# Kernel tuning notes

Measured on AMD Instinct MI355X. Metric: run time of the kernel, lower is better.

## Reference

```python
import jax, jax.numpy as jnp
import numpy as np

N_STATE = 1024
N_HEAD = 16
HEAD_DIM = N_STATE // N_HEAD
SCALE = HEAD_DIM ** (-0.25)


def setup_inputs() -> dict:
    key = jax.random.key(0)
    ks = jax.random.split(key, 9)
    B, S, D = 32, 1500, N_STATE
    std = 1.0 / np.sqrt(D)
    return {
        "hidden_states": jax.random.normal(ks[0], (B, 1, D), dtype=jnp.float32),
        "encoder_output": jax.random.normal(ks[1], (B, S, D), dtype=jnp.float32),
        "Wq": jax.random.normal(ks[2], (D, D), dtype=jnp.float32) * std,
        "bq": jax.random.normal(ks[3], (D,), dtype=jnp.float32) * std,
        "Wk": jax.random.normal(ks[4], (D, D), dtype=jnp.float32) * std,
        "Wv": jax.random.normal(ks[5], (D, D), dtype=jnp.float32) * std,
        "bv": jax.random.normal(ks[6], (D,), dtype=jnp.float32) * std,
        "Wo": jax.random.normal(ks[7], (D, D), dtype=jnp.float32) * std,
        "bo": jax.random.normal(ks[8], (D,), dtype=jnp.float32) * std,
    }


def reference(hidden_states, encoder_output, Wq, bq, Wk, Wv, bv, Wo, bo):
    B = hidden_states.shape[0]
    S = encoder_output.shape[1]
    # projections (torch F.linear: x @ W.T + b)
    q = hidden_states @ Wq.T + bq                  # [B, 1, D]
    k_original = encoder_output @ Wk.T             # [B, S, D] (no bias)
    v_original = encoder_output @ Wv.T + bv        # [B, S, D]

    q = q.reshape(B, 1, N_HEAD, HEAD_DIM).transpose(0, 2, 1, 3)         # [B,H,1,hd]
    k = k_original.reshape(B, S, N_HEAD, HEAD_DIM).transpose(0, 2, 1, 3)  # [B,H,S,hd]
    v = v_original.reshape(B, S, N_HEAD, HEAD_DIM).transpose(0, 2, 1, 3)  # [B,H,S,hd]

    # pre-scaled q and k, scores in fp32 softmax then cast back
    attn_weights = jnp.einsum('bhqd,bhkd->bhqk', q * SCALE, k * SCALE)  # [B,H,1,S]
    attn_weights = jax.nn.softmax(attn_weights.astype(jnp.float32), axis=-1).astype(q.dtype)
    attn_output = jnp.einsum('bhqk,bhkd->bhqd', attn_weights, v)        # [B,H,1,hd]
    attn_output = attn_output.transpose(0, 2, 1, 3).reshape(B, 1, N_STATE)
    attn_output = attn_output @ Wo.T + bo
    return attn_output, k_original, v_original
```

## Files before the change

kernel.cpp:

```cpp
#include <hip/hip_runtime.h>
#include <cstdint>
#include <cstddef>

#define D_MODEL 1024
#define NH      16
#define HD      64
#define B_SZ    32
#define SEQ     1500
#define MROWS   (B_SZ * SEQ)
#define KD      1024
#define NCH     16
#define PSTR    68

typedef __attribute__((ext_vector_type(8))) short bf16x8;
typedef __attribute__((ext_vector_type(4))) float f32x4;
typedef unsigned short u16;

__device__ __forceinline__ u16 f2b(float f) {
  unsigned int x = __float_as_uint(f);
  x = (x + 0x7FFFu + ((x >> 16) & 1u)) >> 16;
  return (u16)x;
}

#define ENC_BLOCKS 3000
#define W_BLOCKS   64
#define QPROJ_BLOCKS 64

__global__ __launch_bounds__(256) void cast_all_q(const float* __restrict__ enc,
                                                  const float* __restrict__ Wk,
                                                  const float* __restrict__ Wv,
                                                  const float* __restrict__ hs,
                                                  const float* __restrict__ Wq,
                                                  const float* __restrict__ bq,
                                                  u16* __restrict__ encb,
                                                  u16* __restrict__ wkvb,
                                                  float* __restrict__ qs) {
  const int tid = threadIdx.x;
  const int bid = blockIdx.x;
  if (bid < ENC_BLOCKS) {
    const float4* s4 = (const float4*)enc;
    const size_t base = (size_t)bid * 256 + tid;
    #pragma unroll
    for (int k = 0; k < 16; ++k) {
      size_t i = base + (size_t)k * (ENC_BLOCKS * 256);
      float4 a = s4[i];
      u16 u[4] = { f2b(a.x), f2b(a.y), f2b(a.z), f2b(a.w) };
      *reinterpret_cast<uint2*>(encb + i * 4) = *reinterpret_cast<const uint2*>(u);
    }
  } else if (bid < ENC_BLOCKS + W_BLOCKS) {
    const int wb = bid - ENC_BLOCKS;
    const size_t base = (size_t)wb * 256 + tid;
    const int NW4 = KD * KD / 4;
    #pragma unroll
    for (int k = 0; k < 32; ++k) {
      size_t i = base + (size_t)k * (W_BLOCKS * 256);
      const float4* s4 = (i < (size_t)NW4) ? (const float4*)Wk : (const float4*)Wv;
      size_t j = (i < (size_t)NW4) ? i : i - NW4;
      float4 a = s4[j];
      u16 u[4] = { f2b(a.x), f2b(a.y), f2b(a.z), f2b(a.w) };
      *reinterpret_cast<uint2*>(wkvb + i * 4) = *reinterpret_cast<const uint2*>(u);
    }
  } else {
    const int qb = bid - ENC_BLOCKS - W_BLOCKS;
    const int n  = qb * 16 + (tid & 15);
    const int bb = tid >> 4;
    const float4* wp  = (const float4*)(Wq + (size_t)n * D_MODEL);
    const float4* x0p = (const float4*)(hs + (size_t)bb * D_MODEL);
    const float4* x1p = (const float4*)(hs + (size_t)(bb + 16) * D_MODEL);
    float a0 = 0.f, a1 = 0.f;
    #pragma unroll 8
    for (int i = 0; i < D_MODEL / 4; ++i) {
      float4 w = wp[i], x0 = x0p[i], x1 = x1p[i];
      a0 += w.x * x0.x + w.y * x0.y + w.z * x0.z + w.w * x0.w;
      a1 += w.x * x1.x + w.y * x1.y + w.z * x1.z + w.w * x1.w;
    }
    const float bqn = bq[n];
    qs[(size_t)bb * D_MODEL + n]        = (a0 + bqn) * 0.125f;
    qs[(size_t)(bb + 16) * D_MODEL + n] = (a1 + bqn) * 0.125f;
  }
}

#define GBM 128
#define GBN 256
#define GBK 32
#define GNT (KD / GBK)
#define AT  (GBM * GBK)
#define BT  (GBN * GBK)

__device__ __forceinline__ void stageA(const u16* __restrict__ Ag, u16* lbuf,
                                       long m0, int kt, int tid) {
  int c = tid;
  int r = c >> 2, cp = c & 3;
  int scp = cp ^ ((r >> 1) & 3);
  const u16* src = Ag + (m0 + r) * (long)KD + kt * GBK + scp * 8;
  __builtin_amdgcn_global_load_lds((const __attribute__((address_space(1))) void*)src,
      (__attribute__((address_space(3))) void*)(lbuf + (size_t)c * 8), 16, 0, 0);
}

__device__ __forceinline__ void stageB(const u16* __restrict__ Bg, u16* lbuf,
                                       int n0, int kt, int tid) {
  #pragma unroll
  for (int L = 0; L < 2; ++L) {
    int c = tid + L * 512;
    int r = c >> 2, cp = c & 3;
    int scp = cp ^ ((r >> 1) & 3);
    const u16* src = Bg + (size_t)(n0 + r) * KD + kt * GBK + scp * 8;
    __builtin_amdgcn_global_load_lds((const __attribute__((address_space(1))) void*)src,
        (__attribute__((address_space(3))) void*)(lbuf + (size_t)c * 8), 16, 0, 0);
  }
}

__device__ __forceinline__ bf16x8 ldFrag(const u16* buf, int row, int lane) {
  int r  = row + (lane & 15);
  int ch = (lane >> 4) ^ ((r >> 1) & 3);
  return *(const bf16x8*)(buf + (size_t)r * GBK + ch * 8);
}

__global__ __launch_bounds__(512, 4) void gemm_kv(const u16* __restrict__ A,
                                                  const u16* __restrict__ Bm,
                                                  const float* __restrict__ bv,
                                                  float* __restrict__ Kout,
                                                  float* __restrict__ Vout) {
  __shared__ __align__(16) char smem[3 * (GBM + GBN) * GBK * 2];
  u16* sAb = (u16*)smem;
  u16* sBb = sAb + 3 * AT;

  const int tid  = threadIdx.x;
  const int lane = tid & 63;
  const int wid  = tid >> 6;
  const int wr   = wid >> 2;
  const int wc   = wid & 3;

  int bx = (blockIdx.x & 7) * (gridDim.x >> 3) + (blockIdx.x >> 3);
  const int  mt = bx >> 3;
  const int  nt = bx & 7;
  const long m0 = (long)mt * GBM;
  const int  n0 = nt * GBN;

  stageA(A, sAb + 0 * AT, m0, 0, tid);
  stageB(Bm, sBb + 0 * BT, n0, 0, tid);
  stageA(A, sAb + 1 * AT, m0, 1, tid);
  stageB(Bm, sBb + 1 * BT, n0, 1, tid);
  stageA(A, sAb + 2 * AT, m0, 2, tid);
  stageB(Bm, sBb + 2 * BT, n0, 2, tid);

  f32x4 acc[4][4] = {};

  for (int t = 0; t < GNT; ++t) {
    if (t < GNT - 2)       { asm volatile("s_waitcnt vmcnt(6)" ::: "memory"); }
    else if (t == GNT - 2) { asm volatile("s_waitcnt vmcnt(3)" ::: "memory"); }
    else                   { asm volatile("s_waitcnt vmcnt(0)" ::: "memory"); }
    __builtin_amdgcn_s_barrier();

    const int  bi = t % 3;
    const u16* cA = sAb + bi * AT;
    const u16* cB = sBb + bi * BT;
    bf16x8 af[4], bfr[4];
    #pragma unroll
    for (int mf = 0; mf < 4; ++mf) af[mf]  = ldFrag(cA, wr * 64 + mf * 16, lane);
    #pragma unroll
    for (int nf = 0; nf < 4; ++nf) bfr[nf] = ldFrag(cB, wc * 64 + nf * 16, lane);
    asm volatile("s_waitcnt lgkmcnt(0)" ::: "memory");
    __builtin_amdgcn_s_barrier();

    if (t + 3 < GNT) {
      stageA(A, sAb + bi * AT, m0, t + 3, tid);
      stageB(Bm, sBb + bi * BT, n0, t + 3, tid);
    }

    #pragma unroll
    for (int mf = 0; mf < 4; ++mf)
      #pragma unroll
      for (int nf = 0; nf < 4; ++nf)
        acc[mf][nf] = __builtin_amdgcn_mfma_f32_16x16x32_bf16(af[mf], bfr[nf], acc[mf][nf], 0, 0, 0);
  }

  __syncthreads();
  float (*ep)[260] = (float(*)[260])smem;

  const bool isV = (nt >= 4);
  float* Co = isV ? Vout : Kout;
  const int ncol0 = isV ? (n0 - 1024) : n0;
  float4 bias4[4];
  #pragma unroll
  for (int k = 0; k < 4; ++k) {
    int c4 = (tid + 512 * k) & 63;
    bias4[k] = isV ? reinterpret_cast<const float4*>(bv)[(ncol0 >> 2) + c4]
                   : make_float4(0.f, 0.f, 0.f, 0.f);
  }

  #pragma unroll
  for (int p = 0; p < 4; ++p) {
    if (wr == (p >> 1)) {
      const int mfb = (p & 1) * 2;
      #pragma unroll
      for (int mm = 0; mm < 2; ++mm)
        #pragma unroll
        for (int nf = 0; nf < 4; ++nf)
          #pragma unroll
          for (int r = 0; r < 4; ++r)
            ep[mm * 16 + (lane >> 4) * 4 + r][wc * 64 + nf * 16 + (lane & 15)] =
                acc[mfb + mm][nf][r];
    }
    __syncthreads();
    #pragma unroll
    for (int k = 0; k < 4; ++k) {
      int idx = tid + 512 * k;
      int row = idx >> 6;
      int c4  = idx & 63;
      long grow = m0 + p * 32 + row;
      float4 v = *reinterpret_cast<const float4*>(&ep[row][c4 * 4]);
      v.x += bias4[k].x; v.y += bias4[k].y; v.z += bias4[k].z; v.w += bias4[k].w;
      *reinterpret_cast<float4*>(&Co[grow * D_MODEL + ncol0 + c4 * 4]) = v;
    }
    __syncthreads();
  }
}

__global__ __launch_bounds__(256) void attn_part(const float* __restrict__ qs,
                                                 const float* __restrict__ K,
                                                 const float* __restrict__ V,
                                                 float* __restrict__ part) {
  const int b = blockIdx.x >> 4;
  const int c = blockIdx.x & 15;
  const int tid = threadIdx.x;
  const int h = tid >> 4;
  const int j = tid & 15;
  const int s0 = (c * SEQ) >> 4;
  const int s1 = (((c + 1) * SEQ) >> 4);

  const float4 q4 = ((const float4*)(qs + (size_t)b * D_MODEL))[tid];
  float m = -1e30f, l = 0.f;
  float4 pv = make_float4(0.f, 0.f, 0.f, 0.f);

  int i = s0;
  for (; i + 2 <= s1; i += 2) {
    const float4 kA = ((const float4*)(K + (size_t)(b * SEQ + i) * D_MODEL))[tid];
    const float4 vA = ((const float4*)(V + (size_t)(b * SEQ + i) * D_MODEL))[tid];
    const float4 kB = ((const float4*)(K + (size_t)(b * SEQ + i + 1) * D_MODEL))[tid];
    const float4 vB = ((const float4*)(V + (size_t)(b * SEQ + i + 1) * D_MODEL))[tid];

    float sA = kA.x * q4.x + kA.y * q4.y + kA.z * q4.z + kA.w * q4.w;
    sA += __shfl_xor(sA, 1); sA += __shfl_xor(sA, 2);
    sA += __shfl_xor(sA, 4); sA += __shfl_xor(sA, 8);
    float mn = fmaxf(m, sA);
    float sc = __expf(m - mn);
    float p  = __expf(sA - mn);
    m = mn;
    l = l * sc + p;
    pv.x = pv.x * sc + p * vA.x; pv.y = pv.y * sc + p * vA.y;
    pv.z = pv.z * sc + p * vA.z; pv.w = pv.w * sc + p * vA.w;

    float sB = kB.x * q4.x + kB.y * q4.y + kB.z * q4.z + kB.w * q4.w;
    sB += __shfl_xor(sB, 1); sB += __shfl_xor(sB, 2);
    sB += __shfl_xor(sB, 4); sB += __shfl_xor(sB, 8);
    mn = fmaxf(m, sB);
    sc = __expf(m - mn);
    p  = __expf(sB - mn);
    m = mn;
    l = l * sc + p;
    pv.x = pv.x * sc + p * vB.x; pv.y = pv.y * sc + p * vB.y;
    pv.z = pv.z * sc + p * vB.z; pv.w = pv.w * sc + p * vB.w;
  }
  if (i < s1) {
    const float4 kA = ((const float4*)(K + (size_t)(b * SEQ + i) * D_MODEL))[tid];
    const float4 vA = ((const float4*)(V + (size_t)(b * SEQ + i) * D_MODEL))[tid];
    float sA = kA.x * q4.x + kA.y * q4.y + kA.z * q4.z + kA.w * q4.w;
    sA += __shfl_xor(sA, 1); sA += __shfl_xor(sA, 2);
    sA += __shfl_xor(sA, 4); sA += __shfl_xor(sA, 8);
    float mn = fmaxf(m, sA);
    float sc = __expf(m - mn);
    float p  = __expf(sA - mn);
    m = mn;
    l = l * sc + p;
    pv.x = pv.x * sc + p * vA.x; pv.y = pv.y * sc + p * vA.y;
    pv.z = pv.z * sc + p * vA.z; pv.w = pv.w * sc + p * vA.w;
  }

  float* pp = part + ((size_t)(b * NH + h) * NCH + c) * PSTR;
  *(float4*)(pp + j * 4) = pv;
  if (j == 0) { pp[64] = m; pp[65] = l; }
}

__global__ __launch_bounds__(256) void oproj_comb(const float* __restrict__ part,
                                                  const float* __restrict__ Wo,
                                                  const float* __restrict__ bo,
                                                  float* __restrict__ out) {
  const int b = blockIdx.x >> 3, ch = blockIdx.x & 7;
  const int tid = threadIdx.x;
  __shared__ float xs[D_MODEL];

  {
    const int h = tid >> 4;
    const int d = (tid & 15) * 4;
    const float* pp = part + (size_t)(b * NH + h) * NCH * PSTR;
    float M = -1e30f;
    #pragma unroll
    for (int cc = 0; cc < NCH; ++cc) M = fmaxf(M, pp[cc * PSTR + 64]);
    float Lsum = 0.f;
    float4 o = make_float4(0.f, 0.f, 0.f, 0.f);
    #pragma unroll
    for (int cc = 0; cc < NCH; ++cc) {
      const float wgt = __expf(pp[cc * PSTR + 64] - M);
      Lsum += pp[cc * PSTR + 65] * wgt;
      float4 pv = *(const float4*)(pp + cc * PSTR + d);
      o.x += pv.x * wgt; o.y += pv.y * wgt; o.z += pv.z * wgt; o.w += pv.w * wgt;
    }
    const float inv = 1.0f / Lsum;
    xs[h * HD + d]     = o.x * inv;
    xs[h * HD + d + 1] = o.y * inv;
    xs[h * HD + d + 2] = o.z * inv;
    xs[h * HD + d + 3] = o.w * inv;
  }
  __syncthreads();

  const int n = ch * 128 + (tid >> 1);
  const int half = tid & 1;
  const float4* wp = (const float4*)(Wo + (size_t)n * D_MODEL + half * 512);
  const float4* xp = (const float4*)xs + half * 128;
  float a = 0.f;
  #pragma unroll 8
  for (int i = 0; i < 128; ++i) {
    float4 w = wp[i], xv = xp[i];
    a += w.x * xv.x + w.y * xv.y + w.z * xv.z + w.w * xv.w;
  }
  a += __shfl_xor(a, 1);
  if (!half) out[(size_t)b * D_MODEL + n] = a + bo[n];
}

extern "C" void kernel_launch(void* const* d_in, const int* in_sizes, int n_in,
                              void* d_out, int out_size, void* d_ws, size_t ws_size,
                              hipStream_t stream) {
  const float* hs  = (const float*)d_in[0];
  const float* enc = (const float*)d_in[1];
  const float* Wq  = (const float*)d_in[2];
  const float* bq  = (const float*)d_in[3];
  const float* Wk  = (const float*)d_in[4];
  const float* Wv  = (const float*)d_in[5];
  const float* bv  = (const float*)d_in[6];
  const float* Wo  = (const float*)d_in[7];
  const float* bo  = (const float*)d_in[8];

  float* out   = (float*)d_out;
  float* attnO = out;
  float* Kout  = out + 32768;
  float* Vout  = Kout + (size_t)MROWS * D_MODEL;

  char* ws = (char*)d_ws;
  const size_t off_wkvb = (size_t)MROWS * D_MODEL * 2;
  const size_t off_qs   = off_wkvb + 4194304;
  const size_t off_part = off_qs + 131072;

  u16*   encb = (u16*)ws;
  u16*   wkvb = (u16*)(ws + off_wkvb);
  float* qs   = (float*)(ws + off_qs);
  float* part = (float*)(ws + off_part);

  cast_all_q<<<ENC_BLOCKS + W_BLOCKS + QPROJ_BLOCKS, 256, 0, stream>>>(enc, Wk, Wv, hs, Wq, bq,
                                                                       encb, wkvb, qs);

  gemm_kv<<<(MROWS / GBM) * (2048 / GBN), 512, 0, stream>>>(encb, wkvb, bv, Kout, Vout);

  attn_part<<<B_SZ * NCH, 256, 0, stream>>>(qs, Kout, Vout, part);
  oproj_comb<<<B_SZ * 8, 256, 0, stream>>>(part, Wo, bo, attnO);
}
```

Before: 440.4 us.

## Split attention into more sequence chunks with dual online-softmax accumulators

Raises the number of sequence chunks per batch in the decode attention kernel from 16 to 64, so 2048 blocks stream K/V instead of 512. Inside each block, two independent online-softmax accumulators replace the serial chain and are merged at the end, increasing instruction-level parallelism. The combine step moves into its own kernel, the partials reuse the no-longer-needed bf16 encoder workspace, and the output projection becomes a separate kernel. This adds a third kernel launch and more partial data to combine.

```diff
diff --git a/kernel.cpp b/kernel.cpp
--- a/kernel.cpp
+++ b/kernel.cpp
@@ -9,7 +9,7 @@
 #define SEQ     1500
 #define MROWS   (B_SZ * SEQ)
 #define KD      1024
-#define NCH     16
+#define NCH     64
 #define PSTR    68
 
 typedef __attribute__((ext_vector_type(8))) short bf16x8;
@@ -221,17 +221,18 @@
                                                  const float* __restrict__ K,
                                                  const float* __restrict__ V,
                                                  float* __restrict__ part) {
-  const int b = blockIdx.x >> 4;
-  const int c = blockIdx.x & 15;
+  const int b = blockIdx.x >> 6;
+  const int c = blockIdx.x & 63;
   const int tid = threadIdx.x;
   const int h = tid >> 4;
   const int j = tid & 15;
-  const int s0 = (c * SEQ) >> 4;
-  const int s1 = (((c + 1) * SEQ) >> 4);
+  const int s0 = (c * SEQ) >> 6;
+  const int s1 = ((c + 1) * SEQ) >> 6;
 
   const float4 q4 = ((const float4*)(qs + (size_t)b * D_MODEL))[tid];
-  float m = -1e30f, l = 0.f;
-  float4 pv = make_float4(0.f, 0.f, 0.f, 0.f);
+  float mA = -1e30f, lA = 0.f, mB = -1e30f, lB = 0.f;
+  float4 pvA = make_float4(0.f, 0.f, 0.f, 0.f);
+  float4 pvB = make_float4(0.f, 0.f, 0.f, 0.f);
 
   int i = s0;
   for (; i + 2 <= s1; i += 2) {
@@ -241,26 +242,21 @@
     const float4 vB = ((const float4*)(V + (size_t)(b * SEQ + i + 1) * D_MODEL))[tid];
 
     float sA = kA.x * q4.x + kA.y * q4.y + kA.z * q4.z + kA.w * q4.w;
-    sA += __shfl_xor(sA, 1); sA += __shfl_xor(sA, 2);
-    sA += __shfl_xor(sA, 4); sA += __shfl_xor(sA, 8);
-    float mn = fmaxf(m, sA);
-    float sc = __expf(m - mn);
-    float p  = __expf(sA - mn);
-    m = mn;
-    l = l * sc + p;
-    pv.x = pv.x * sc + p * vA.x; pv.y = pv.y * sc + p * vA.y;
-    pv.z = pv.z * sc + p * vA.z; pv.w = pv.w * sc + p * vA.w;
-
     float sB = kB.x * q4.x + kB.y * q4.y + kB.z * q4.z + kB.w * q4.w;
-    sB += __shfl_xor(sB, 1); sB += __shfl_xor(sB, 2);
-    sB += __shfl_xor(sB, 4); sB += __shfl_xor(sB, 8);
-    mn = fmaxf(m, sB);
-    sc = __expf(m - mn);
-    p  = __expf(sB - mn);
-    m = mn;
-    l = l * sc + p;
-    pv.x = pv.x * sc + p * vB.x; pv.y = pv.y * sc + p * vB.y;
-    pv.z = pv.z * sc + p * vB.z; pv.w = pv.w * sc + p * vB.w;
+    sA += __shfl_xor(sA, 1); sB += __shfl_xor(sB, 1);
+    sA += __shfl_xor(sA, 2); sB += __shfl_xor(sB, 2);
+    sA += __shfl_xor(sA, 4); sB += __shfl_xor(sB, 4);
+    sA += __shfl_xor(sA, 8); sB += __shfl_xor(sB, 8);
+
+    float mnA = fmaxf(mA, sA), mnB = fmaxf(mB, sB);
+    float scA = __expf(mA - mnA), scB = __expf(mB - mnB);
+    float pA  = __expf(sA - mnA), pB  = __expf(sB - mnB);
+    mA = mnA; mB = mnB;
+    lA = lA * scA + pA; lB = lB * scB + pB;
+    pvA.x = pvA.x * scA + pA * vA.x; pvB.x = pvB.x * scB + pB * vB.x;
+    pvA.y = pvA.y * scA + pA * vA.y; pvB.y = pvB.y * scB + pB * vB.y;
+    pvA.z = pvA.z * scA + pA * vA.z; pvB.z = pvB.z * scB + pB * vB.z;
+    pvA.w = pvA.w * scA + pA * vA.w; pvB.w = pvB.w * scB + pB * vB.w;
   }
   if (i < s1) {
     const float4 kA = ((const float4*)(K + (size_t)(b * SEQ + i) * D_MODEL))[tid];
@@ -268,52 +264,57 @@
     float sA = kA.x * q4.x + kA.y * q4.y + kA.z * q4.z + kA.w * q4.w;
     sA += __shfl_xor(sA, 1); sA += __shfl_xor(sA, 2);
     sA += __shfl_xor(sA, 4); sA += __shfl_xor(sA, 8);
-    float mn = fmaxf(m, sA);
-    float sc = __expf(m - mn);
+    float mn = fmaxf(mA, sA);
+    float sc = __expf(mA - mn);
     float p  = __expf(sA - mn);
-    m = mn;
-    l = l * sc + p;
-    pv.x = pv.x * sc + p * vA.x; pv.y = pv.y * sc + p * vA.y;
-    pv.z = pv.z * sc + p * vA.z; pv.w = pv.w * sc + p * vA.w;
-  }
+    mA = mn;
+    lA = lA * sc + p;
+    pvA.x = pvA.x * sc + p * vA.x; pvA.y = pvA.y * sc + p * vA.y;
+    pvA.z = pvA.z * sc + p * vA.z; pvA.w = pvA.w * sc + p * vA.w;
+  }
+
+  const float m = fmaxf(mA, mB);
+  const float wA = __expf(mA - m), wB = __expf(mB - m);
+  const float l = lA * wA + lB * wB;
+  float4 pv;
+  pv.x = pvA.x * wA + pvB.x * wB;
+  pv.y = pvA.y * wA + pvB.y * wB;
+  pv.z = pvA.z * wA + pvB.z * wB;
+  pv.w = pvA.w * wA + pvB.w * wB;
 
   float* pp = part + ((size_t)(b * NH + h) * NCH + c) * PSTR;
   *(float4*)(pp + j * 4) = pv;
   if (j == 0) { pp[64] = m; pp[65] = l; }
 }
 
-__global__ __launch_bounds__(256) void oproj_comb(const float* __restrict__ part,
-                                                  const float* __restrict__ Wo,
-                                                  const float* __restrict__ bo,
-                                                  float* __restrict__ out) {
+__global__ __launch_bounds__(64) void attn_comb(const float* __restrict__ part,
+                                                float* __restrict__ attnc) {
+  const int bh = blockIdx.x;
+  const int b = bh >> 4, h = bh & 15;
+  const int tid = threadIdx.x;
+  const float* pp = part + (size_t)bh * NCH * PSTR;
+  float M = -1e30f;
+  #pragma unroll 8
+  for (int c = 0; c < NCH; ++c) M = fmaxf(M, pp[c * PSTR + 64]);
+  float L = 0.f, o = 0.f;
+  #pragma unroll 8
+  for (int c = 0; c < NCH; ++c) {
+    const float w = __expf(pp[c * PSTR + 64] - M);
+    L += pp[c * PSTR + 65] * w;
+    o += pp[c * PSTR + tid] * w;
+  }
+  attnc[(size_t)b * D_MODEL + h * HD + tid] = o / L;
+}
+
+__global__ __launch_bounds__(256) void oproj_kernel(const float* __restrict__ x,
+                                                    const float* __restrict__ Wo,
+                                                    const float* __restrict__ bo,
+                                                    float* __restrict__ out) {
   const int b = blockIdx.x >> 3, ch = blockIdx.x & 7;
   const int tid = threadIdx.x;
   __shared__ float xs[D_MODEL];
-
-  {
-    const int h = tid >> 4;
-    const int d = (tid & 15) * 4;
-    const float* pp = part + (size_t)(b * NH + h) * NCH * PSTR;
-    float M = -1e30f;
-    #pragma unroll
-    for (int cc = 0; cc < NCH; ++cc) M = fmaxf(M, pp[cc * PSTR + 64]);
-    float Lsum = 0.f;
-    float4 o = make_float4(0.f, 0.f, 0.f, 0.f);
-    #pragma unroll
-    for (int cc = 0; cc < NCH; ++cc) {
-      const float wgt = __expf(pp[cc * PSTR + 64] - M);
-      Lsum += pp[cc * PSTR + 65] * wgt;
-      float4 pv = *(const float4*)(pp + cc * PSTR + d);
-      o.x += pv.x * wgt; o.y += pv.y * wgt; o.z += pv.z * wgt; o.w += pv.w * wgt;
-    }
-    const float inv = 1.0f / Lsum;
-    xs[h * HD + d]     = o.x * inv;
-    xs[h * HD + d + 1] = o.y * inv;
-    xs[h * HD + d + 2] = o.z * inv;
-    xs[h * HD + d + 3] = o.w * inv;
-  }
+  ((float4*)xs)[tid] = ((const float4*)(x + (size_t)b * D_MODEL))[tid];
   __syncthreads();
-
   const int n = ch * 128 + (tid >> 1);
   const int half = tid & 1;
   const float4* wp = (const float4*)(Wo + (size_t)n * D_MODEL + half * 512);
@@ -349,12 +350,13 @@
   char* ws = (char*)d_ws;
   const size_t off_wkvb = (size_t)MROWS * D_MODEL * 2;
   const size_t off_qs   = off_wkvb + 4194304;
-  const size_t off_part = off_qs + 131072;
-
-  u16*   encb = (u16*)ws;
-  u16*   wkvb = (u16*)(ws + off_wkvb);
-  float* qs   = (float*)(ws + off_qs);
-  float* part = (float*)(ws + off_part);
+  const size_t off_attnc= off_qs + 131072;
+
+  u16*   encb  = (u16*)ws;
+  float* part  = (float*)ws;
+  u16*   wkvb  = (u16*)(ws + off_wkvb);
+  float* qs    = (float*)(ws + off_qs);
+  float* attnc = (float*)(ws + off_attnc);
 
   cast_all_q<<<ENC_BLOCKS + W_BLOCKS + QPROJ_BLOCKS, 256, 0, stream>>>(enc, Wk, Wv, hs, Wq, bq,
                                                                        encb, wkvb, qs);
@@ -362,5 +364,6 @@
   gemm_kv<<<(MROWS / GBM) * (2048 / GBN), 512, 0, stream>>>(encb, wkvb, bv, Kout, Vout);
 
   attn_part<<<B_SZ * NCH, 256, 0, stream>>>(qs, Kout, Vout, part);
-  oproj_comb<<<B_SZ * 8, 256, 0, stream>>>(part, Wo, bo, attnO);
-}
+  attn_comb<<<B_SZ * NH, 64, 0, stream>>>(part, attnc);
+  oproj_kernel<<<B_SZ * 8, 256, 0, stream>>>(attnc, Wo, bo, attnO);
+}
```

Result: slower. 458.4 us (+4.1%).

## Fuse fp32-to-bf16 encoder cast into GEMM A-tile loads

Applied to the files above, without the earlier changes.

The separate pass that converted the whole encoder output to bf16 is removed. The K/V GEMM now stages fp32 A tiles straight into LDS and converts them to bf16 with v_cvt_pk_bf16_f32 when loading fragments. This drops a full read and write of the large bf16 intermediate. In exchange, each N-tile block re-reads fp32 A at twice the bytes, and LDS per stage grows, so the pipeline goes from triple to double buffering. Conversion work also now runs inside the GEMM inner loop.

```diff
diff --git a/kernel.cpp b/kernel.cpp
--- a/kernel.cpp
+++ b/kernel.cpp
@@ -22,34 +22,26 @@
   return (u16)x;
 }
 
-#define ENC_BLOCKS 3000
+__device__ __forceinline__ unsigned cvtpk(float lo, float hi) {
+  unsigned r;
+  asm("v_cvt_pk_bf16_f32 %0, %1, %2" : "=v"(r) : "v"(lo), "v"(hi));
+  return r;
+}
+
 #define W_BLOCKS   64
 #define QPROJ_BLOCKS 64
 
-__global__ __launch_bounds__(256) void cast_all_q(const float* __restrict__ enc,
-                                                  const float* __restrict__ Wk,
-                                                  const float* __restrict__ Wv,
-                                                  const float* __restrict__ hs,
-                                                  const float* __restrict__ Wq,
-                                                  const float* __restrict__ bq,
-                                                  u16* __restrict__ encb,
-                                                  u16* __restrict__ wkvb,
-                                                  float* __restrict__ qs) {
+__global__ __launch_bounds__(256) void prep_kernel(const float* __restrict__ Wk,
+                                                   const float* __restrict__ Wv,
+                                                   const float* __restrict__ hs,
+                                                   const float* __restrict__ Wq,
+                                                   const float* __restrict__ bq,
+                                                   u16* __restrict__ wkvb,
+                                                   float* __restrict__ qs) {
   const int tid = threadIdx.x;
   const int bid = blockIdx.x;
-  if (bid < ENC_BLOCKS) {
-    const float4* s4 = (const float4*)enc;
+  if (bid < W_BLOCKS) {
     const size_t base = (size_t)bid * 256 + tid;
-    #pragma unroll
-    for (int k = 0; k < 16; ++k) {
-      size_t i = base + (size_t)k * (ENC_BLOCKS * 256);
-      float4 a = s4[i];
-      u16 u[4] = { f2b(a.x), f2b(a.y), f2b(a.z), f2b(a.w) };
-      *reinterpret_cast<uint2*>(encb + i * 4) = *reinterpret_cast<const uint2*>(u);
-    }
-  } else if (bid < ENC_BLOCKS + W_BLOCKS) {
-    const int wb = bid - ENC_BLOCKS;
-    const size_t base = (size_t)wb * 256 + tid;
     const int NW4 = KD * KD / 4;
     #pragma unroll
     for (int k = 0; k < 32; ++k) {
@@ -61,7 +53,7 @@
       *reinterpret_cast<uint2*>(wkvb + i * 4) = *reinterpret_cast<const uint2*>(u);
     }
   } else {
-    const int qb = bid - ENC_BLOCKS - W_BLOCKS;
+    const int qb = bid - W_BLOCKS;
     const int n  = qb * 16 + (tid & 15);
     const int bb = tid >> 4;
     const float4* wp  = (const float4*)(Wq + (size_t)n * D_MODEL);
@@ -84,17 +76,20 @@
 #define GBN 256
 #define GBK 32
 #define GNT (KD / GBK)
-#define AT  (GBM * GBK)
-#define BT  (GBN * GBK)
-
-__device__ __forceinline__ void stageA(const u16* __restrict__ Ag, u16* lbuf,
+#define ATF (GBM * GBK)
+#define BTU (GBN * GBK)
+
+__device__ __forceinline__ void stageA(const float* __restrict__ Ag, float* lbuf,
                                        long m0, int kt, int tid) {
-  int c = tid;
-  int r = c >> 2, cp = c & 3;
-  int scp = cp ^ ((r >> 1) & 3);
-  const u16* src = Ag + (m0 + r) * (long)KD + kt * GBK + scp * 8;
-  __builtin_amdgcn_global_load_lds((const __attribute__((address_space(1))) void*)src,
-      (__attribute__((address_space(3))) void*)(lbuf + (size_t)c * 8), 16, 0, 0);
+  #pragma unroll
+  for (int L = 0; L < 2; ++L) {
+    int c = tid + L * 512;
+    int r = c >> 3, cp = c & 7;
+    int scp = cp ^ (r & 7);
+    const float* src = Ag + (m0 + r) * (long)KD + kt * GBK + scp * 4;
+    __builtin_amdgcn_global_load_lds((const __attribute__((address_space(1))) void*)src,
+        (__attribute__((address_space(3))) void*)(lbuf + (size_t)c * 4), 16, 0, 0);
+  }
 }
 
 __device__ __forceinline__ void stageB(const u16* __restrict__ Bg, u16* lbuf,
@@ -110,20 +105,37 @@
   }
 }
 
-__device__ __forceinline__ bf16x8 ldFrag(const u16* buf, int row, int lane) {
+__device__ __forceinline__ bf16x8 ldFragA(const float* buf, int row, int lane) {
+  int r  = row + (lane & 15);
+  int k0 = lane >> 4;
+  int c0 = (2 * k0)     ^ (r & 7);
+  int c1 = (2 * k0 + 1) ^ (r & 7);
+  f32x4 lo = *(const f32x4*)(buf + (size_t)r * GBK + c0 * 4);
+  f32x4 hi = *(const f32x4*)(buf + (size_t)r * GBK + c1 * 4);
+  unsigned u0 = cvtpk(lo[0], lo[1]);
+  unsigned u1 = cvtpk(lo[2], lo[3]);
+  unsigned u2 = cvtpk(hi[0], hi[1]);
+  unsigned u3 = cvtpk(hi[2], hi[3]);
+  unsigned v[4] = { u0, u1, u2, u3 };
+  return *reinterpret_cast<const bf16x8*>(v);
+}
+
+__device__ __forceinline__ bf16x8 ldFragB(const u16* buf, int row, int lane) {
   int r  = row + (lane & 15);
   int ch = (lane >> 4) ^ ((r >> 1) & 3);
   return *(const bf16x8*)(buf + (size_t)r * GBK + ch * 8);
 }
 
-__global__ __launch_bounds__(512, 4) void gemm_kv(const u16* __restrict__ A,
+__global__ __launch_bounds__(512, 4) void gemm_kv(const float* __restrict__ A,
                                                   const u16* __restrict__ Bm,
                                                   const float* __restrict__ bv,
                                                   float* __restrict__ Kout,
                                                   float* __restrict__ Vout) {
-  __shared__ __align__(16) char smem[3 * (GBM + GBN) * GBK * 2];
-  u16* sAb = (u16*)smem;
-  u16* sBb = sAb + 3 * AT;
+  __shared__ __align__(16) char smem[2 * ATF * 4 + 2 * BTU * 2];
+  float* sA0 = (float*)smem;
+  float* sA1 = sA0 + ATF;
+  u16*   sB0 = (u16*)(sA1 + ATF);
+  u16*   sB1 = sB0 + BTU;
 
   const int tid  = threadIdx.x;
   const int lane = tid & 63;
@@ -137,35 +149,33 @@
   const long m0 = (long)mt * GBM;
   const int  n0 = nt * GBN;
 
-  stageA(A, sAb + 0 * AT, m0, 0, tid);
-  stageB(Bm, sBb + 0 * BT, n0, 0, tid);
-  stageA(A, sAb + 1 * AT, m0, 1, tid);
-  stageB(Bm, sBb + 1 * BT, n0, 1, tid);
-  stageA(A, sAb + 2 * AT, m0, 2, tid);
-  stageB(Bm, sBb + 2 * BT, n0, 2, tid);
+  stageA(A, sA0, m0, 0, tid);
+  stageB(Bm, sB0, n0, 0, tid);
+  stageA(A, sA1, m0, 1, tid);
+  stageB(Bm, sB1, n0, 1, tid);
 
   f32x4 acc[4][4] = {};
 
   for (int t = 0; t < GNT; ++t) {
-    if (t < GNT - 2)       { asm volatile("s_waitcnt vmcnt(6)" ::: "memory"); }
-    else if (t == GNT - 2) { asm volatile("s_waitcnt vmcnt(3)" ::: "memory"); }
-    else                   { asm volatile("s_waitcnt vmcnt(0)" ::: "memory"); }
+    if (t == GNT - 1) { asm volatile("s_waitcnt vmcnt(0)" ::: "memory"); }
+    else              { asm volatile("s_waitcnt vmcnt(4)" ::: "memory"); }
     __builtin_amdgcn_s_barrier();
 
-    const int  bi = t % 3;
-    const u16* cA = sAb + bi * AT;
-    const u16* cB = sBb + bi * BT;
+    const float* cA = (t & 1) ? sA1 : sA0;
+    const u16*   cB = (t & 1) ? sB1 : sB0;
     bf16x8 af[4], bfr[4];
     #pragma unroll
-    for (int mf = 0; mf < 4; ++mf) af[mf]  = ldFrag(cA, wr * 64 + mf * 16, lane);
-    #pragma unroll
-    for (int nf = 0; nf < 4; ++nf) bfr[nf] = ldFrag(cB, wc * 64 + nf * 16, lane);
+    for (int mf = 0; mf < 4; ++mf) af[mf]  = ldFragA(cA, wr * 64 + mf * 16, lane);
+    #pragma unroll
+    for (int nf = 0; nf < 4; ++nf) bfr[nf] = ldFragB(cB, wc * 64 + nf * 16, lane);
     asm volatile("s_waitcnt lgkmcnt(0)" ::: "memory");
     __builtin_amdgcn_s_barrier();
 
-    if (t + 3 < GNT) {
-      stageA(A, sAb + bi * AT, m0, t + 3, tid);
-      stageB(Bm, sBb + bi * BT, n0, t + 3, tid);
+    if (t + 2 < GNT) {
+      float* pA = (t & 1) ? sA1 : sA0;
+      u16*   pB = (t & 1) ? sB1 : sB0;
+      stageA(A, pA, m0, t + 2, tid);
+      stageB(Bm, pB, n0, t + 2, tid);
     }
 
     #pragma unroll
@@ -347,19 +357,13 @@
   float* Vout  = Kout + (size_t)MROWS * D_MODEL;
 
   char* ws = (char*)d_ws;
-  const size_t off_wkvb = (size_t)MROWS * D_MODEL * 2;
-  const size_t off_qs   = off_wkvb + 4194304;
-  const size_t off_part = off_qs + 131072;
-
-  u16*   encb = (u16*)ws;
-  u16*   wkvb = (u16*)(ws + off_wkvb);
-  float* qs   = (float*)(ws + off_qs);
-  float* part = (float*)(ws + off_part);
-
-  cast_all_q<<<ENC_BLOCKS + W_BLOCKS + QPROJ_BLOCKS, 256, 0, stream>>>(enc, Wk, Wv, hs, Wq, bq,
-                                                                       encb, wkvb, qs);
-
-  gemm_kv<<<(MROWS / GBM) * (2048 / GBN), 512, 0, stream>>>(encb, wkvb, bv, Kout, Vout);
+  u16*   wkvb = (u16*)ws;
+  float* qs   = (float*)(ws + 4194304);
+  float* part = (float*)(ws + 4194304 + 131072);
+
+  prep_kernel<<<W_BLOCKS + QPROJ_BLOCKS, 256, 0, stream>>>(Wk, Wv, hs, Wq, bq, wkvb, qs);
+
+  gemm_kv<<<(MROWS / GBM) * (2048 / GBN), 512, 0, stream>>>(enc, wkvb, bv, Kout, Vout);
 
   attn_part<<<B_SZ * NCH, 256, 0, stream>>>(qs, Kout, Vout, part);
   oproj_comb<<<B_SZ * 8, 256, 0, stream>>>(part, Wo, bo, attnO);
```

New measurement: 464.1 us. 1.05x slower.
